# Kernel tuning notes

Hardware: AMD Instinct MI355X
Metric: run time of the kernel (lower is better)

The kernel has to match this reference:

```python
import jax, jax.numpy as jnp
import numpy as np

NUM_HEADS = 12

def setup_inputs() -> dict:
    key = jax.random.key(0)
    ks = jax.random.split(key, 6)
    B, N, C = 8, 1024, 768
    x = jax.random.normal(ks[0], (B, N, C), dtype=jnp.float32)
    qkv_w = jax.random.normal(ks[1], (3 * C, C), dtype=jnp.float32) * 0.02
    qkv_b = jax.random.normal(ks[2], (3 * C,), dtype=jnp.float32) * 0.02
    static_a = jax.random.normal(ks[3], (1, NUM_HEADS, N, N), dtype=jnp.float32) * 0.02
    proj_w = jax.random.normal(ks[4], (C, C), dtype=jnp.float32) * 0.02
    proj_b = jax.random.normal(ks[5], (C,), dtype=jnp.float32) * 0.02
    return {"x": x, "qkv_w": qkv_w, "qkv_b": qkv_b, "static_a": static_a,
            "proj_w": proj_w, "proj_b": proj_b}

def reference(x, qkv_w, qkv_b, static_a, proj_w, proj_b):
    B, N, C = x.shape
    H = NUM_HEADS
    D = C // H
    scale = D ** -0.5
    # qkv: [B,N,3C] -> [3,B,H,N,D]
    qkv = (x @ qkv_w.T + qkv_b).reshape(B, N, 3, H, D).transpose(2, 0, 3, 1, 4)
    q, k, v = qkv[0], qkv[1], qkv[2]
    attn = jnp.einsum('bhnd,bhmd->bhnm', q, k) * scale
    attn = jax.nn.softmax(attn, axis=-1)
    attn = attn + static_a  # static bias added AFTER softmax (no renorm)
    out = jnp.einsum('bhnm,bhmd->bhnd', attn, v)  # [B,H,N,D]
    out = out.transpose(0, 2, 1, 3).reshape(B, N, C)
    return out @ proj_w.T + proj_b
```

## Files before the change

kernel.cpp:

```cpp
#include <hip/hip_runtime.h>
#include <math.h>

#define NB   8
#define SEQ  1024
#define CH   768
#define NH   12
#define HD   64
#define BHT  (NB * NH)
#define QKVN 2304

typedef unsigned short u16;
typedef unsigned int   u32;
typedef __attribute__((ext_vector_type(8))) short bf16x8;
typedef __attribute__((ext_vector_type(4))) float f32x4;

__device__ __forceinline__ float bf2f(u32 s) {
    union { u32 u; float f; } v; v.u = s << 16; return v.f;
}
__device__ __forceinline__ u16 f2bf(float f) {
    union { float f; u32 u; } v; v.f = f;
    u32 u = v.u;
    return (u16)((u + 0x7fffu + ((u >> 16) & 1u)) >> 16);
}
__device__ __forceinline__ float ld1(const u16* p) { return bf2f((u32)*p); }
__device__ __forceinline__ void st1(u16* p, float v) { *p = f2bf(v); }
__device__ __forceinline__ void st1(float* p, float v) { *p = v; }

__global__ void detect_kernel(const u32* __restrict__ x, int* __restrict__ flag) {
    __shared__ int cnt;
    if (threadIdx.x == 0) cnt = 0;
    __syncthreads();
    int c = 0;
    for (int i = threadIdx.x; i < 2048; i += 256) {
        const u32 e0 = (x[i] >> 7) & 0xFFu;
        c += (e0 >= 110u && e0 <= 132u) ? 1 : 0;
    }
    atomicAdd(&cnt, c);
    __syncthreads();
    if (threadIdx.x == 0) *flag = (cnt > 1024) ? 1 : 0;
}

#define PREP_V4 5309184
__device__ __forceinline__ void prep_seg(size_t v, const void* const s[6],
                                         const size_t e0[6], int* segp, size_t* offp) {
    int seg = 5;
    if      (v < 1572864) seg = 0;
    else if (v < 2015232) seg = 1;
    else if (v < 2015808) seg = 2;
    else if (v < 5161536) seg = 3;
    else if (v < 5308992) seg = 4;
    *segp = seg; *offp = v * 4 - e0[seg];
}

__global__ __launch_bounds__(256) void prep_f32(
    const int* __restrict__ flag,
    const float* __restrict__ s0, const float* __restrict__ s1, const float* __restrict__ s2,
    const float* __restrict__ s3, const float* __restrict__ s4, const float* __restrict__ s5,
    u16* __restrict__ dst)
{
    if (*flag != 0) return;
    const void* const srcs[6] = {s0, s1, s2, s3, s4, s5};
    const size_t e0[6] = {0, 6291456, 8060928, 8063232, 20646144, 21235968};
    for (size_t v = blockIdx.x * 256 + threadIdx.x; v < PREP_V4; v += (size_t)gridDim.x * 256) {
        int seg; size_t off;
        prep_seg(v, srcs, e0, &seg, &off);
        const float4 f = *(const float4*)((const float*)srcs[seg] + off);
        ushort4 o; o.x = f2bf(f.x); o.y = f2bf(f.y); o.z = f2bf(f.z); o.w = f2bf(f.w);
        *(ushort4*)(dst + v * 4) = o;
    }
}

__global__ __launch_bounds__(256) void prep_bf16(
    const int* __restrict__ flag,
    const u16* __restrict__ s0, const u16* __restrict__ s1, const u16* __restrict__ s2,
    const u16* __restrict__ s3, const u16* __restrict__ s4, const u16* __restrict__ s5,
    u16* __restrict__ dst)
{
    if (*flag != 1) return;
    const void* const srcs[6] = {s0, s1, s2, s3, s4, s5};
    const size_t e0[6] = {0, 6291456, 8060928, 8063232, 20646144, 21235968};
    for (size_t v = blockIdx.x * 256 + threadIdx.x; v < PREP_V4; v += (size_t)gridDim.x * 256) {
        int seg; size_t off;
        prep_seg(v, srcs, e0, &seg, &off);
        *(ushort4*)(dst + v * 4) = *(const ushort4*)((const u16*)srcs[seg] + off);
    }
}

__device__ __forceinline__ void gemm128_core(
    const u16* __restrict__ Ag, const u16* __restrict__ Bg,
    f32x4 acc[4][4], u16* As, u16* Bs, int wm, int wn, int l15, int quad)
{
    const int t = threadIdx.x;
    const int srow = t >> 1, shalf = (t & 1) * 16;
#pragma unroll
    for (int mi = 0; mi < 4; mi++)
#pragma unroll
        for (int ni = 0; ni < 4; ni++) { f32x4 z = {0.f,0.f,0.f,0.f}; acc[mi][ni] = z; }

    for (int k0 = 0; k0 < CH; k0 += 32) {
        const uint4 a0 = *(const uint4*)(Ag + k0);
        const uint4 a1 = *(const uint4*)(Ag + k0 + 8);
        const uint4 b0 = *(const uint4*)(Bg + k0);
        const uint4 b1 = *(const uint4*)(Bg + k0 + 8);
        __syncthreads();
        u16* da = &As[srow * 40 + shalf];
        u16* db = &Bs[srow * 40 + shalf];
        *(uint4*)da = a0; *(uint4*)(da + 8) = a1;
        *(uint4*)db = b0; *(uint4*)(db + 8) = b1;
        __syncthreads();
        bf16x8 af[4], bfr[4];
#pragma unroll
        for (int mi = 0; mi < 4; mi++)
            af[mi] = *(const bf16x8*)&As[(wm * 64 + mi * 16 + l15) * 40 + quad * 8];
#pragma unroll
        for (int ni = 0; ni < 4; ni++)
            bfr[ni] = *(const bf16x8*)&Bs[(wn * 64 + ni * 16 + l15) * 40 + quad * 8];
#pragma unroll
        for (int mi = 0; mi < 4; mi++)
#pragma unroll
            for (int ni = 0; ni < 4; ni++)
                acc[mi][ni] = __builtin_amdgcn_mfma_f32_16x16x32_bf16(
                    af[mi], bfr[ni], acc[mi][ni], 0, 0, 0);
    }
}

__global__ __launch_bounds__(256) void qkv_gemm(
    const u16* __restrict__ x, const u16* __restrict__ w, const u16* __restrict__ bias,
    u16* __restrict__ Qn, u16* __restrict__ Kn, u16* __restrict__ Vt)
{
    __shared__ u16 As[128 * 40];
    __shared__ u16 Bs[128 * 40];
    const int t = threadIdx.x;
    const int lane = t & 63, wv = t >> 6;
    const int l15 = lane & 15, quad = lane >> 4;
    const int wm = wv >> 1, wn = wv & 1;
    const int m0 = blockIdx.y * 128, n0 = blockIdx.x * 128;
    const int srow = t >> 1, shalf = (t & 1) * 16;

    f32x4 acc[4][4];
    gemm128_core(x + (size_t)(m0 + srow) * CH + shalf,
                 w + (size_t)(n0 + srow) * CH + shalf,
                 acc, As, Bs, wm, wn, l15, quad);

    const int which = n0 / CH;
    const int h     = (n0 % CH) / HD + wn;
    const float qsc = (which == 0) ? 0.125f : 1.0f;
    float bv[4];
#pragma unroll
    for (int ni = 0; ni < 4; ni++) bv[ni] = ld1(bias + n0 + wn * 64 + ni * 16 + l15);

#pragma unroll
    for (int mi = 0; mi < 4; mi++) {
        const int mg   = m0 + wm * 64 + mi * 16 + quad * 4;
        const int b    = mg >> 10, seq0 = mg & 1023;
        const size_t bh = (size_t)b * NH + h;
#pragma unroll
        for (int ni = 0; ni < 4; ni++) {
            const int d = ni * 16 + l15;
            float v[4];
#pragma unroll
            for (int r = 0; r < 4; r++) v[r] = (acc[mi][ni][r] + bv[ni]) * qsc;
            if (which == 2) {
                ushort4 o; o.x=f2bf(v[0]); o.y=f2bf(v[1]); o.z=f2bf(v[2]); o.w=f2bf(v[3]);
                *(ushort4*)&Vt[(bh * HD + d) * SEQ + seq0] = o;
            } else {
                u16* dst = ((which == 0) ? Qn : Kn) + (bh * SEQ + seq0) * HD + d;
#pragma unroll
                for (int r = 0; r < 4; r++) dst[(size_t)r * HD] = f2bf(v[r]);
            }
        }
    }
}

__global__ __launch_bounds__(256) void attn_kernel(
    const u16* __restrict__ Qn, const u16* __restrict__ Kn, const u16* __restrict__ Vt,
    const u16* __restrict__ Ab, u16* __restrict__ AO)
{
    __shared__ u16 Ks[64 * 72];
    __shared__ u16 Vs[64 * 72];
    __shared__ u16 Ps[4 * 32 * 72];

    const int qb = blockIdx.x;
    const int bh = blockIdx.y;
    const int hh = bh % NH, b = bh / NH;
    const int t  = threadIdx.x;
    const int w  = t >> 6, lane = t & 63;
    const int l15 = lane & 15, quad = lane >> 4;
    const int sr = t >> 2, sc = (t & 3) * 16;
    const int i0g = qb * 128 + w * 32;
    u16* Psw = Ps + w * 32 * 72;

    bf16x8 qa[2][2];
#pragma unroll
    for (int isub = 0; isub < 2; isub++)
#pragma unroll
        for (int db = 0; db < 2; db++)
            qa[isub][db] = *(const bf16x8*)(Qn +
                ((size_t)bh * SEQ + i0g + isub * 16 + l15) * HD + db * 32 + quad * 8);

    f32x4 Op[2][4], Oa[2][4];
#pragma unroll
    for (int i = 0; i < 2; i++)
#pragma unroll
        for (int d = 0; d < 4; d++) { f32x4 z = {0.f,0.f,0.f,0.f}; Op[i][d] = z; Oa[i][d] = z; }
    float rl[2][4] = {{0.f,0.f,0.f,0.f},{0.f,0.f,0.f,0.f}};

    for (int kt = 0; kt < 16; kt++) {
        const int j0 = kt * 64;
        bf16x8 afr[2][2];
#pragma unroll
        for (int jb = 0; jb < 2; jb++)
#pragma unroll
            for (int isub = 0; isub < 2; isub++)
                afr[jb][isub] = *(const bf16x8*)(Ab +
                    ((size_t)hh * SEQ + i0g + isub * 16 + l15) * SEQ
                    + j0 + jb * 32 + quad * 8);

        const u16* kp = Kn + ((size_t)bh * SEQ + j0 + sr) * HD + sc;
        const u16* vp = Vt + ((size_t)bh * HD + sr) * SEQ + j0 + sc;
        const uint4 k0v = *(const uint4*)kp, k1v = *(const uint4*)(kp + 8);
        const uint4 v0v = *(const uint4*)vp, v1v = *(const uint4*)(vp + 8);
        __syncthreads();
        *(uint4*)&Ks[sr * 72 + sc] = k0v; *(uint4*)&Ks[sr * 72 + sc + 8] = k1v;
        *(uint4*)&Vs[sr * 72 + sc] = v0v; *(uint4*)&Vs[sr * 72 + sc + 8] = v1v;
        __syncthreads();

#pragma unroll
        for (int j16 = 0; j16 < 4; j16++) {
            const bf16x8 kf0 = *(const bf16x8*)&Ks[(j16 * 16 + l15) * 72 + quad * 8];
            const bf16x8 kf1 = *(const bf16x8*)&Ks[(j16 * 16 + l15) * 72 + 32 + quad * 8];
#pragma unroll
            for (int isub = 0; isub < 2; isub++) {
                f32x4 s = {0.f, 0.f, 0.f, 0.f};
                s = __builtin_amdgcn_mfma_f32_16x16x32_bf16(qa[isub][0], kf0, s, 0, 0, 0);
                s = __builtin_amdgcn_mfma_f32_16x16x32_bf16(qa[isub][1], kf1, s, 0, 0, 0);
#pragma unroll
                for (int r = 0; r < 4; r++) {
                    const float p = __expf(fminf(s[r], 60.f));
                    rl[isub][r] += p;
                    Psw[(isub * 16 + quad * 4 + r) * 72 + j16 * 16 + l15] = f2bf(p);
                }
            }
        }

#pragma unroll
        for (int jb = 0; jb < 2; jb++) {
            bf16x8 pf[2];
#pragma unroll
            for (int isub = 0; isub < 2; isub++)
                pf[isub] = *(const bf16x8*)&Psw[(isub * 16 + l15) * 72 + jb * 32 + quad * 8];
#pragma unroll
            for (int d16 = 0; d16 < 4; d16++) {
                const bf16x8 vf = *(const bf16x8*)&Vs[(d16 * 16 + l15) * 72 + jb * 32 + quad * 8];
#pragma unroll
                for (int isub = 0; isub < 2; isub++) {
                    Op[isub][d16] = __builtin_amdgcn_mfma_f32_16x16x32_bf16(pf[isub], vf, Op[isub][d16], 0, 0, 0);
                    Oa[isub][d16] = __builtin_amdgcn_mfma_f32_16x16x32_bf16(afr[jb][isub], vf, Oa[isub][d16], 0, 0, 0);
                }
            }
        }
    }

#pragma unroll
    for (int isub = 0; isub < 2; isub++)
#pragma unroll
        for (int r = 0; r < 4; r++) {
            float v = rl[isub][r];
            v += __shfl_xor(v, 1); v += __shfl_xor(v, 2);
            v += __shfl_xor(v, 4); v += __shfl_xor(v, 8);
            rl[isub][r] = 1.f / v;
        }
#pragma unroll
    for (int isub = 0; isub < 2; isub++)
#pragma unroll
        for (int d16 = 0; d16 < 4; d16++)
#pragma unroll
            for (int r = 0; r < 4; r++) {
                const int n = i0g + isub * 16 + quad * 4 + r;
                const float v = Op[isub][d16][r] * rl[isub][r] + Oa[isub][d16][r];
                AO[((size_t)b * SEQ + n) * CH + hh * HD + d16 * 16 + l15] = f2bf(v);
            }
}

template<typename TO>
__global__ __launch_bounds__(256) void proj_gemm(
    const int* __restrict__ flag, const int want,
    const u16* __restrict__ AO, const u16* __restrict__ w, const u16* __restrict__ bias,
    TO* __restrict__ out)
{
    if (*flag != want) return;
    __shared__ u16 As[128 * 40];
    __shared__ u16 Bs[128 * 40];
    const int t = threadIdx.x;
    const int lane = t & 63, wv = t >> 6;
    const int l15 = lane & 15, quad = lane >> 4;
    const int wm = wv >> 1, wn = wv & 1;
    const int m0 = blockIdx.y * 128, n0 = blockIdx.x * 128;
    const int srow = t >> 1, shalf = (t & 1) * 16;

    f32x4 acc[4][4];
    gemm128_core(AO + (size_t)(m0 + srow) * CH + shalf,
                 w  + (size_t)(n0 + srow) * CH + shalf,
                 acc, As, Bs, wm, wn, l15, quad);

    float bv[4];
#pragma unroll
    for (int ni = 0; ni < 4; ni++) bv[ni] = ld1(bias + n0 + wn * 64 + ni * 16 + l15);
#pragma unroll
    for (int mi = 0; mi < 4; mi++) {
        const int mg = m0 + wm * 64 + mi * 16 + quad * 4;
#pragma unroll
        for (int ni = 0; ni < 4; ni++)
#pragma unroll
            for (int r = 0; r < 4; r++)
                st1(out + (size_t)(mg + r) * CH + n0 + wn * 64 + ni * 16 + l15,
                    acc[mi][ni][r] + bv[ni]);
    }
}

extern "C" void kernel_launch(void* const* d_in, const int* in_sizes, int n_in,
                              void* d_out, int out_size, void* d_ws, size_t ws_size,
                              hipStream_t stream) {
    (void)in_sizes; (void)n_in; (void)out_size; (void)ws_size;
    u16* ws = (u16*)d_ws;
    u16* xb   = ws;
    u16* wqb  = ws + 6291456;
    u16* bqb  = ws + 8060928;
    u16* Ab   = ws + 8063232;
    u16* pwb  = ws + 20646144;
    u16* pbb  = ws + 21235968;
    u16* arena_end = ws + 21236736;
    const size_t S1 = (size_t)NB * NH * SEQ * HD;
    u16* Qn = arena_end;
    u16* Kn = Qn + S1;
    u16* Vt = Kn + S1;
    u16* AO = Vt + S1;
    int* flag = (int*)(AO + S1);

    detect_kernel<<<dim3(1), dim3(256), 0, stream>>>((const u32*)d_in[0], flag);

    const dim3 blk(256);
    prep_f32 <<<dim3(4096), blk, 0, stream>>>(flag,
        (const float*)d_in[0], (const float*)d_in[1], (const float*)d_in[2],
        (const float*)d_in[3], (const float*)d_in[4], (const float*)d_in[5], ws);
    prep_bf16<<<dim3(4096), blk, 0, stream>>>(flag,
        (const u16*)d_in[0], (const u16*)d_in[1], (const u16*)d_in[2],
        (const u16*)d_in[3], (const u16*)d_in[4], (const u16*)d_in[5], ws);

    qkv_gemm<<<dim3(QKVN / 128, (NB * SEQ) / 128), blk, 0, stream>>>(
        xb, wqb, bqb, Qn, Kn, Vt);
    attn_kernel<<<dim3(SEQ / 128, BHT), blk, 0, stream>>>(Qn, Kn, Vt, Ab, AO);

    proj_gemm<float><<<dim3(CH / 128, (NB * SEQ) / 128), blk, 0, stream>>>(
        flag, 0, AO, pwb, pbb, (float*)d_out);
    proj_gemm<u16><<<dim3(CH / 128, (NB * SEQ) / 128), blk, 0, stream>>>(
        flag, 1, AO, pwb, pbb, (u16*)d_out);
}
```

Before: 305.9 us.

## Use direct global-to-LDS loads with swizzle and vectorized transposed epilogue stores

The shared GEMM core now loads tiles with global_load_lds straight into an unpadded, XOR-rotated LDS layout instead of staging through registers. MFMA operands are swapped so output rows sit per lane, which lets the QKV, attention and projection epilogues write 4-wide vector stores in place of scalar strided ones. The attention grid is also remapped so blocks sharing a head are adjacent, which may help L2 reuse of the static bias. The cost is extra shuffles to redistribute row sums and the reliance on a synchronous LDS-DMA path with no prefetching.

```diff
diff --git a/kernel.cpp b/kernel.cpp
--- a/kernel.cpp
+++ b/kernel.cpp
@@ -25,6 +25,19 @@
 __device__ __forceinline__ float ld1(const u16* p) { return bf2f((u32)*p); }
 __device__ __forceinline__ void st1(u16* p, float v) { *p = f2bf(v); }
 __device__ __forceinline__ void st1(float* p, float v) { *p = v; }
+__device__ __forceinline__ void st4v(u16* p, float a, float b, float c, float d) {
+    ushort4 o; o.x = f2bf(a); o.y = f2bf(b); o.z = f2bf(c); o.w = f2bf(d);
+    *(ushort4*)p = o;
+}
+__device__ __forceinline__ void st4v(float* p, float a, float b, float c, float d) {
+    float4 o; o.x = a; o.y = b; o.z = c; o.w = d;
+    *(float4*)p = o;
+}
+__device__ __forceinline__ void gload16(const u16* g, u16* l) {
+    __builtin_amdgcn_global_load_lds(
+        (const __attribute__((address_space(1))) void*)g,
+        (__attribute__((address_space(3))) void*)l, 16, 0, 0);
+}
 
 __global__ void detect_kernel(const u32* __restrict__ x, int* __restrict__ flag) {
     __shared__ int cnt;
@@ -41,8 +54,8 @@
 }
 
 #define PREP_V4 5309184
-__device__ __forceinline__ void prep_seg(size_t v, const void* const s[6],
-                                         const size_t e0[6], int* segp, size_t* offp) {
+__device__ __forceinline__ void prep_seg(size_t v, const size_t e0[6],
+                                         int* segp, size_t* offp) {
     int seg = 5;
     if      (v < 1572864) seg = 0;
     else if (v < 2015232) seg = 1;
@@ -59,12 +72,12 @@
     u16* __restrict__ dst)
 {
     if (*flag != 0) return;
-    const void* const srcs[6] = {s0, s1, s2, s3, s4, s5};
+    const float* const srcs[6] = {s0, s1, s2, s3, s4, s5};
     const size_t e0[6] = {0, 6291456, 8060928, 8063232, 20646144, 21235968};
     for (size_t v = blockIdx.x * 256 + threadIdx.x; v < PREP_V4; v += (size_t)gridDim.x * 256) {
         int seg; size_t off;
-        prep_seg(v, srcs, e0, &seg, &off);
-        const float4 f = *(const float4*)((const float*)srcs[seg] + off);
+        prep_seg(v, e0, &seg, &off);
+        const float4 f = *(const float4*)(srcs[seg] + off);
         ushort4 o; o.x = f2bf(f.x); o.y = f2bf(f.y); o.z = f2bf(f.z); o.w = f2bf(f.w);
         *(ushort4*)(dst + v * 4) = o;
     }
@@ -77,50 +90,65 @@
     u16* __restrict__ dst)
 {
     if (*flag != 1) return;
-    const void* const srcs[6] = {s0, s1, s2, s3, s4, s5};
+    const u16* const srcs[6] = {s0, s1, s2, s3, s4, s5};
     const size_t e0[6] = {0, 6291456, 8060928, 8063232, 20646144, 21235968};
     for (size_t v = blockIdx.x * 256 + threadIdx.x; v < PREP_V4; v += (size_t)gridDim.x * 256) {
         int seg; size_t off;
-        prep_seg(v, srcs, e0, &seg, &off);
-        *(ushort4*)(dst + v * 4) = *(const ushort4*)((const u16*)srcs[seg] + off);
-    }
-}
-
+        prep_seg(v, e0, &seg, &off);
+        *(ushort4*)(dst + v * 4) = *(const ushort4*)(srcs[seg] + off);
+    }
+}
+
+template<bool SWAP>
 __device__ __forceinline__ void gemm128_core(
     const u16* __restrict__ Ag, const u16* __restrict__ Bg,
     f32x4 acc[4][4], u16* As, u16* Bs, int wm, int wn, int l15, int quad)
 {
     const int t = threadIdx.x;
-    const int srow = t >> 1, shalf = (t & 1) * 16;
+    const int w = t >> 6, lane = t & 63;
+    const int lr = lane >> 2, lc = lane & 3;
+    const int r0 = w * 16 + lr;
+    const int r1 = 64 + w * 16 + lr;
+    const int g0 = (lc + r0) & 3, g1 = (lc + r1) & 3;
+    const u16* a0 = Ag + (size_t)r0 * CH + g0 * 8;
+    const u16* a1 = Ag + (size_t)r1 * CH + g1 * 8;
+    const u16* b0 = Bg + (size_t)r0 * CH + g0 * 8;
+    const u16* b1 = Bg + (size_t)r1 * CH + g1 * 8;
+    u16* lA0 = As + w * 512;
+    u16* lA1 = As + 2048 + w * 512;
+    u16* lB0 = Bs + w * 512;
+    u16* lB1 = Bs + 2048 + w * 512;
+
 #pragma unroll
     for (int mi = 0; mi < 4; mi++)
 #pragma unroll
         for (int ni = 0; ni < 4; ni++) { f32x4 z = {0.f,0.f,0.f,0.f}; acc[mi][ni] = z; }
 
     for (int k0 = 0; k0 < CH; k0 += 32) {
-        const uint4 a0 = *(const uint4*)(Ag + k0);
-        const uint4 a1 = *(const uint4*)(Ag + k0 + 8);
-        const uint4 b0 = *(const uint4*)(Bg + k0);
-        const uint4 b1 = *(const uint4*)(Bg + k0 + 8);
         __syncthreads();
-        u16* da = &As[srow * 40 + shalf];
-        u16* db = &Bs[srow * 40 + shalf];
-        *(uint4*)da = a0; *(uint4*)(da + 8) = a1;
-        *(uint4*)db = b0; *(uint4*)(db + 8) = b1;
+        gload16(a0 + k0, lA0);
+        gload16(a1 + k0, lA1);
+        gload16(b0 + k0, lB0);
+        gload16(b1 + k0, lB1);
         __syncthreads();
         bf16x8 af[4], bfr[4];
 #pragma unroll
+        for (int mi = 0; mi < 4; mi++) {
+            const int ra = wm * 64 + mi * 16 + l15;
+            af[mi] = *(const bf16x8*)&As[ra * 32 + ((quad - ra) & 3) * 8];
+        }
+#pragma unroll
+        for (int ni = 0; ni < 4; ni++) {
+            const int rb = wn * 64 + ni * 16 + l15;
+            bfr[ni] = *(const bf16x8*)&Bs[rb * 32 + ((quad - rb) & 3) * 8];
+        }
+#pragma unroll
         for (int mi = 0; mi < 4; mi++)
-            af[mi] = *(const bf16x8*)&As[(wm * 64 + mi * 16 + l15) * 40 + quad * 8];
-#pragma unroll
-        for (int ni = 0; ni < 4; ni++)
-            bfr[ni] = *(const bf16x8*)&Bs[(wn * 64 + ni * 16 + l15) * 40 + quad * 8];
-#pragma unroll
-        for (int mi = 0; mi < 4; mi++)
 #pragma unroll
             for (int ni = 0; ni < 4; ni++)
-                acc[mi][ni] = __builtin_amdgcn_mfma_f32_16x16x32_bf16(
-                    af[mi], bfr[ni], acc[mi][ni], 0, 0, 0);
+                acc[mi][ni] = SWAP
+                    ? __builtin_amdgcn_mfma_f32_16x16x32_bf16(bfr[ni], af[mi], acc[mi][ni], 0, 0, 0)
+                    : __builtin_amdgcn_mfma_f32_16x16x32_bf16(af[mi], bfr[ni], acc[mi][ni], 0, 0, 0);
     }
 }
 
@@ -128,45 +156,58 @@
     const u16* __restrict__ x, const u16* __restrict__ w, const u16* __restrict__ bias,
     u16* __restrict__ Qn, u16* __restrict__ Kn, u16* __restrict__ Vt)
 {
-    __shared__ u16 As[128 * 40];
-    __shared__ u16 Bs[128 * 40];
-    const int t = threadIdx.x;
-    const int lane = t & 63, wv = t >> 6;
+    __shared__ u16 As[128 * 32];
+    __shared__ u16 Bs[128 * 32];
+    const int t = threadIdx.x, lane = t & 63, wv = t >> 6;
     const int l15 = lane & 15, quad = lane >> 4;
     const int wm = wv >> 1, wn = wv & 1;
     const int m0 = blockIdx.y * 128, n0 = blockIdx.x * 128;
-    const int srow = t >> 1, shalf = (t & 1) * 16;
-
+    const int which = n0 / CH;
+    const int h     = ((n0 % CH) >> 6) + wn;
+    const int b     = m0 >> 10;
+    const size_t bh = (size_t)b * NH + h;
+    const int sq0   = m0 & 1023;
     f32x4 acc[4][4];
-    gemm128_core(x + (size_t)(m0 + srow) * CH + shalf,
-                 w + (size_t)(n0 + srow) * CH + shalf,
-                 acc, As, Bs, wm, wn, l15, quad);
-
-    const int which = n0 / CH;
-    const int h     = (n0 % CH) / HD + wn;
-    const float qsc = (which == 0) ? 0.125f : 1.0f;
-    float bv[4];
-#pragma unroll
-    for (int ni = 0; ni < 4; ni++) bv[ni] = ld1(bias + n0 + wn * 64 + ni * 16 + l15);
-
-#pragma unroll
-    for (int mi = 0; mi < 4; mi++) {
-        const int mg   = m0 + wm * 64 + mi * 16 + quad * 4;
-        const int b    = mg >> 10, seq0 = mg & 1023;
-        const size_t bh = (size_t)b * NH + h;
-#pragma unroll
-        for (int ni = 0; ni < 4; ni++) {
-            const int d = ni * 16 + l15;
-            float v[4];
-#pragma unroll
-            for (int r = 0; r < 4; r++) v[r] = (acc[mi][ni][r] + bv[ni]) * qsc;
-            if (which == 2) {
-                ushort4 o; o.x=f2bf(v[0]); o.y=f2bf(v[1]); o.z=f2bf(v[2]); o.w=f2bf(v[3]);
-                *(ushort4*)&Vt[(bh * HD + d) * SEQ + seq0] = o;
-            } else {
-                u16* dst = ((which == 0) ? Qn : Kn) + (bh * SEQ + seq0) * HD + d;
-#pragma unroll
-                for (int r = 0; r < 4; r++) dst[(size_t)r * HD] = f2bf(v[r]);
+
+    if (which == 2) {
+        gemm128_core<false>(x + (size_t)m0 * CH, w + (size_t)n0 * CH,
+                            acc, As, Bs, wm, wn, l15, quad);
+        float bv[4];
+#pragma unroll
+        for (int ni = 0; ni < 4; ni++) bv[ni] = ld1(bias + n0 + wn * 64 + ni * 16 + l15);
+#pragma unroll
+        for (int mi = 0; mi < 4; mi++) {
+            const int seq = sq0 + wm * 64 + mi * 16 + quad * 4;
+#pragma unroll
+            for (int ni = 0; ni < 4; ni++) {
+                const int d = ni * 16 + l15;
+                st4v(&Vt[(bh * HD + d) * SEQ + seq],
+                     acc[mi][ni][0] + bv[ni], acc[mi][ni][1] + bv[ni],
+                     acc[mi][ni][2] + bv[ni], acc[mi][ni][3] + bv[ni]);
+            }
+        }
+    } else {
+        gemm128_core<true>(x + (size_t)m0 * CH, w + (size_t)n0 * CH,
+                           acc, As, Bs, wm, wn, l15, quad);
+        u16* T2 = which ? Kn : Qn;
+        const float qsc = which ? 1.0f : 0.125f;
+        float bvr[4][4];
+#pragma unroll
+        for (int ni = 0; ni < 4; ni++)
+#pragma unroll
+            for (int r = 0; r < 4; r++)
+                bvr[ni][r] = ld1(bias + n0 + wn * 64 + ni * 16 + quad * 4 + r);
+#pragma unroll
+        for (int mi = 0; mi < 4; mi++) {
+            const int seq = sq0 + wm * 64 + mi * 16 + l15;
+#pragma unroll
+            for (int ni = 0; ni < 4; ni++) {
+                const int dbase = ni * 16 + quad * 4;
+                st4v(&T2[(bh * SEQ + seq) * HD + dbase],
+                     (acc[mi][ni][0] + bvr[ni][0]) * qsc,
+                     (acc[mi][ni][1] + bvr[ni][1]) * qsc,
+                     (acc[mi][ni][2] + bvr[ni][2]) * qsc,
+                     (acc[mi][ni][3] + bvr[ni][3]) * qsc);
             }
         }
     }
@@ -181,8 +222,9 @@
     __shared__ u16 Ps[4 * 32 * 72];
 
     const int qb = blockIdx.x;
-    const int bh = blockIdx.y;
-    const int hh = bh % NH, b = bh / NH;
+    const int y  = blockIdx.y;
+    const int hh = y >> 3, b = y & 7;
+    const size_t bh = (size_t)b * NH + hh;
     const int t  = threadIdx.x;
     const int w  = t >> 6, lane = t & 63;
     const int l15 = lane & 15, quad = lane >> 4;
@@ -196,7 +238,7 @@
 #pragma unroll
         for (int db = 0; db < 2; db++)
             qa[isub][db] = *(const bf16x8*)(Qn +
-                ((size_t)bh * SEQ + i0g + isub * 16 + l15) * HD + db * 32 + quad * 8);
+                (bh * SEQ + i0g + isub * 16 + l15) * HD + db * 32 + quad * 8);
 
     f32x4 Op[2][4], Oa[2][4];
 #pragma unroll
@@ -216,8 +258,8 @@
                     ((size_t)hh * SEQ + i0g + isub * 16 + l15) * SEQ
                     + j0 + jb * 32 + quad * 8);
 
-        const u16* kp = Kn + ((size_t)bh * SEQ + j0 + sr) * HD + sc;
-        const u16* vp = Vt + ((size_t)bh * HD + sr) * SEQ + j0 + sc;
+        const u16* kp = Kn + (bh * SEQ + j0 + sr) * HD + sc;
+        const u16* vp = Vt + (bh * HD + sr) * SEQ + j0 + sc;
         const uint4 k0v = *(const uint4*)kp, k1v = *(const uint4*)(kp + 8);
         const uint4 v0v = *(const uint4*)vp, v1v = *(const uint4*)(vp + 8);
         __syncthreads();
@@ -254,32 +296,42 @@
                 const bf16x8 vf = *(const bf16x8*)&Vs[(d16 * 16 + l15) * 72 + jb * 32 + quad * 8];
 #pragma unroll
                 for (int isub = 0; isub < 2; isub++) {
-                    Op[isub][d16] = __builtin_amdgcn_mfma_f32_16x16x32_bf16(pf[isub], vf, Op[isub][d16], 0, 0, 0);
-                    Oa[isub][d16] = __builtin_amdgcn_mfma_f32_16x16x32_bf16(afr[jb][isub], vf, Oa[isub][d16], 0, 0, 0);
+                    Op[isub][d16] = __builtin_amdgcn_mfma_f32_16x16x32_bf16(vf, pf[isub], Op[isub][d16], 0, 0, 0);
+                    Oa[isub][d16] = __builtin_amdgcn_mfma_f32_16x16x32_bf16(vf, afr[jb][isub], Oa[isub][d16], 0, 0, 0);
                 }
             }
         }
     }
 
-#pragma unroll
-    for (int isub = 0; isub < 2; isub++)
+    float inv[2];
+#pragma unroll
+    for (int isub = 0; isub < 2; isub++) {
+        float rr[4];
 #pragma unroll
         for (int r = 0; r < 4; r++) {
             float v = rl[isub][r];
             v += __shfl_xor(v, 1); v += __shfl_xor(v, 2);
             v += __shfl_xor(v, 4); v += __shfl_xor(v, 8);
-            rl[isub][r] = 1.f / v;
-        }
-#pragma unroll
-    for (int isub = 0; isub < 2; isub++)
+            rr[r] = v;
+        }
+        const int src = (l15 >> 2) << 4;
+        const float t0 = __shfl(rr[0], src), t1 = __shfl(rr[1], src);
+        const float t2 = __shfl(rr[2], src), t3 = __shfl(rr[3], src);
+        const float sel = (l15 & 2) ? ((l15 & 1) ? t3 : t2)
+                                    : ((l15 & 1) ? t1 : t0);
+        inv[isub] = 1.f / sel;
+    }
+#pragma unroll
+    for (int isub = 0; isub < 2; isub++) {
+        const int n = i0g + isub * 16 + l15;
 #pragma unroll
         for (int d16 = 0; d16 < 4; d16++)
-#pragma unroll
-            for (int r = 0; r < 4; r++) {
-                const int n = i0g + isub * 16 + quad * 4 + r;
-                const float v = Op[isub][d16][r] * rl[isub][r] + Oa[isub][d16][r];
-                AO[((size_t)b * SEQ + n) * CH + hh * HD + d16 * 16 + l15] = f2bf(v);
-            }
+            st4v(&AO[((size_t)b * SEQ + n) * CH + hh * HD + d16 * 16 + quad * 4],
+                 Op[isub][d16][0] * inv[isub] + Oa[isub][d16][0],
+                 Op[isub][d16][1] * inv[isub] + Oa[isub][d16][1],
+                 Op[isub][d16][2] * inv[isub] + Oa[isub][d16][2],
+                 Op[isub][d16][3] * inv[isub] + Oa[isub][d16][3]);
+    }
 }
 
 template<typename TO>
@@ -289,32 +341,33 @@
     TO* __restrict__ out)
 {
     if (*flag != want) return;
-    __shared__ u16 As[128 * 40];
-    __shared__ u16 Bs[128 * 40];
-    const int t = threadIdx.x;
-    const int lane = t & 63, wv = t >> 6;
+    __shared__ u16 As[128 * 32];
+    __shared__ u16 Bs[128 * 32];
+    const int t = threadIdx.x, lane = t & 63, wv = t >> 6;
     const int l15 = lane & 15, quad = lane >> 4;
     const int wm = wv >> 1, wn = wv & 1;
     const int m0 = blockIdx.y * 128, n0 = blockIdx.x * 128;
-    const int srow = t >> 1, shalf = (t & 1) * 16;
 
     f32x4 acc[4][4];
-    gemm128_core(AO + (size_t)(m0 + srow) * CH + shalf,
-                 w  + (size_t)(n0 + srow) * CH + shalf,
-                 acc, As, Bs, wm, wn, l15, quad);
-
-    float bv[4];
-#pragma unroll
-    for (int ni = 0; ni < 4; ni++) bv[ni] = ld1(bias + n0 + wn * 64 + ni * 16 + l15);
+    gemm128_core<true>(AO + (size_t)m0 * CH, w + (size_t)n0 * CH,
+                       acc, As, Bs, wm, wn, l15, quad);
+
+    float bvr[4][4];
+#pragma unroll
+    for (int ni = 0; ni < 4; ni++)
+#pragma unroll
+        for (int r = 0; r < 4; r++)
+            bvr[ni][r] = ld1(bias + n0 + wn * 64 + ni * 16 + quad * 4 + r);
 #pragma unroll
     for (int mi = 0; mi < 4; mi++) {
-        const int mg = m0 + wm * 64 + mi * 16 + quad * 4;
-#pragma unroll
-        for (int ni = 0; ni < 4; ni++)
-#pragma unroll
-            for (int r = 0; r < 4; r++)
-                st1(out + (size_t)(mg + r) * CH + n0 + wn * 64 + ni * 16 + l15,
-                    acc[mi][ni][r] + bv[ni]);
+        const int m = m0 + wm * 64 + mi * 16 + l15;
+#pragma unroll
+        for (int ni = 0; ni < 4; ni++) {
+            const int n = n0 + wn * 64 + ni * 16 + quad * 4;
+            st4v(out + (size_t)m * CH + n,
+                 acc[mi][ni][0] + bvr[ni][0], acc[mi][ni][1] + bvr[ni][1],
+                 acc[mi][ni][2] + bvr[ni][2], acc[mi][ni][3] + bvr[ni][3]);
+        }
     }
 }
 
```

New measurement: 281.2 us. 1.09x faster.
